# Performance work log

Measured on AMD Instinct MI355X. Metric: run time of the kernel, lower is better.

Reference implementation:

```python
import jax, jax.numpy as jnp
import numpy as np

B, N, K = 32, 1024, 20          # graphs, points per graph, kNN neighbors
EMB = 1024                       # emb_dims
OUT = 7                          # out_channels
WS1, ST1, G1 = 52, 20, 7         # linear1 STFT-KAN: window, stride, gridsize
WS2, ST2, G2 = 197, 7, 6         # linear2 STFT-KAN
NW1 = (128 - WS1) // ST1 + 1     # 4 windows over 128-dim features
NW2 = (2 * EMB - WS2) // ST2 + 1 # 265 windows over 2048-dim features


def _window(kind, M):
    n = jnp.arange(M, dtype=jnp.float32)
    if kind == 'bartlett':
        return 1.0 - jnp.abs(2.0 * n / M - 1.0)        # periodic bartlett (torch default)
    return 0.5 * (1.0 - jnp.cos(2.0 * jnp.pi * n / M)) # periodic hann


def _stft_kan(x, coeffs, bias, gridsize, ws, stride, wtype):
    """x: [B, D]; coeffs: [2, outdim, nw, ws, gridsize]; returns [B, outdim]."""
    D = x.shape[1]
    nw = (D - ws) // stride + 1
    idx = jnp.arange(nw)[:, None] * stride + jnp.arange(ws)[None, :]  # [nw, ws]
    xw = x[:, idx] * _window(wtype, ws)                               # [B, nw, ws]
    kk = jnp.arange(1, gridsize + 1, dtype=x.dtype)
    ang = xw[..., None] * kk                                          # [B, nw, ws, g]
    y = jnp.einsum('bnwg,onwg->bo', jnp.cos(ang), coeffs[0])
    y = y + jnp.einsum('bnwg,onwg->bo', jnp.sin(ang), coeffs[1])
    return y + bias


def setup_inputs() -> dict:
    key = jax.random.key(0)
    ks = jax.random.split(key, 8)
    pos = jax.random.normal(ks[0], (B * N, 3), jnp.float32)
    batch = jnp.repeat(jnp.arange(B, dtype=jnp.int32), N)  # sorted, equal-size graphs
    # EdgeConv MLP([6,64,128]): Linear+BN+ReLU, then plain Linear
    W1 = jax.random.normal(ks[1], (6, 64), jnp.float32) * 0.3
    b1 = jnp.zeros((64,), jnp.float32)
    gamma1 = jnp.ones((64,), jnp.float32)
    beta1 = jnp.zeros((64,), jnp.float32)
    W2 = jax.random.normal(ks[2], (64, 128), jnp.float32) * 0.1
    b2 = jnp.zeros((128,), jnp.float32)
    # STFT-KAN 1 (smooth init: coeffs damped by k^2)
    k1 = np.arange(1, G1 + 1, dtype=np.float32)
    c1 = jax.random.normal(ks[3], (2, EMB, NW1, WS1, G1), jnp.float32) / (np.sqrt(NW1 * WS1) * (k1 ** 2))
    bi1 = jnp.zeros((EMB,), jnp.float32)
    # STFT-KAN 2 (non-smooth init)
    c2 = jax.random.normal(ks[4], (2, OUT, NW2, WS2, G2), jnp.float32) / (np.sqrt(NW2 * WS2) * np.sqrt(G2))
    bi2 = jnp.zeros((OUT,), jnp.float32)
    return {"pos": pos, "batch": batch, "W1": W1, "b1": b1, "gamma1": gamma1,
            "beta1": beta1, "W2": W2, "b2": b2, "c1": c1, "bi1": bi1, "c2": c2, "bi2": bi2}


def reference(pos, batch, W1, b1, gamma1, beta1, W2, b2, c1, bi1, c2, bi2):
    p = pos.reshape(B, N, 3)
    # dynamic kNN graph per batch element (exclude self)
    sq = jnp.sum(p * p, axis=-1)                                    # [B, N]
    d2 = sq[:, :, None] + sq[:, None, :] - 2.0 * jnp.einsum('bnd,bmd->bnm', p, p)
    d2 = d2 + jnp.eye(N, dtype=p.dtype) * 1e10
    _, idx = jax.lax.top_k(-d2, K)                                  # [B, N, K]
    pj = jax.vmap(lambda pts, ids: pts[ids])(p, idx)                # [B, N, K, 3]
    pi = jnp.broadcast_to(p[:, :, None, :], (B, N, K, 3))
    e = jnp.concatenate([pi, pj - pi], axis=-1)                     # [B, N, K, 6]
    # edge MLP: Linear -> BN -> ReLU -> Linear
    h = e @ W1 + b1
    mu = h.mean((0, 1, 2))
    var = h.var((0, 1, 2))
    h = gamma1 * (h - mu) * jax.lax.rsqrt(var + 1e-5) + beta1
    h = jax.nn.relu(h)
    h = h @ W2 + b2                                                 # [B, N, K, 128]
    x1 = h.max(axis=2).reshape(B * N, 128)                          # max aggregation over neighbors
    x = _stft_kan(x1, c1, bi1, G1, WS1, ST1, 'bartlett')            # [B*N, EMB]
    xg = x.reshape(B, N, EMB)
    xcat = jnp.concatenate([xg.max(axis=1), xg.mean(axis=1)], axis=-1)  # global max/mean pool
    return _stft_kan(xcat, c2, bi2, G2, WS2, ST2, 'hann')           # [B, OUT]
```

## Files before the change

kernel.cpp:

```cpp
#include <hip/hip_runtime.h>
#include <cstdint>

typedef _Float16 half8 __attribute__((ext_vector_type(8)));
typedef __fp16 fp16x2 __attribute__((ext_vector_type(2)));
typedef float f32x2 __attribute__((ext_vector_type(2)));
typedef float f32x4 __attribute__((ext_vector_type(4)));

__device__ __forceinline__ void gload16(const void* g, void* l) {
  __builtin_amdgcn_global_load_lds(
      (const __attribute__((address_space(1))) void*)g,
      (__attribute__((address_space(3))) void*)l, 16, 0, 0);
}

__global__ __launch_bounds__(256) void knn_kernel(const float* __restrict__ pos,
                                                  int* __restrict__ nbr) {
  __shared__ float px[1024], py[1024], pz[1024], sq[1024];
  int tid = threadIdx.x;
  int b = blockIdx.x >> 8;
  const float* pg = pos + (size_t)b * 3072;
  for (int m = 0; m < 4; ++m) {
    int j = m * 256 + tid;
    float x = pg[3 * j], y = pg[3 * j + 1], z = pg[3 * j + 2];
    px[j] = x; py[j] = y; pz[j] = z; sq[j] = x * x + y * y + z * z;
  }
  __syncthreads();
  int wave = tid >> 6, lane = tid & 63;
  int n = (blockIdx.x & 255) * 4 + wave;
  float xi = px[n], yi = py[n], zi = pz[n], si = sq[n];
  float d[16];
#pragma unroll
  for (int i = 0; i < 16; ++i) {
    int j = i * 64 + lane;
    float dd = si + sq[j] - 2.0f * (xi * px[j] + yi * py[j] + zi * pz[j]);
    d[i] = (j == n) ? 1e30f : dd;
  }
  int outbase = (b * 1024 + n) * 20;
  for (int kk = 0; kk < 20; ++kk) {
    float lmin = d[0]; int lpos = 0;
#pragma unroll
    for (int i = 1; i < 16; ++i)
      if (d[i] < lmin) { lmin = d[i]; lpos = i; }
    float bv = lmin; int bi = lpos * 64 + lane;
#pragma unroll
    for (int off = 1; off < 64; off <<= 1) {
      float ov = __shfl_xor(bv, off);
      int   oi = __shfl_xor(bi, off);
      if (ov < bv || (ov == bv && oi < bi)) { bv = ov; bi = oi; }
    }
    if (lane == 0) nbr[outbase + kk] = b * 1024 + bi;
    if ((bi & 63) == lane) {
      int rp = bi >> 6;
#pragma unroll
      for (int i = 0; i < 16; ++i)
        if (i == rp) d[i] = 1e30f;
    }
  }
}

__global__ __launch_bounds__(256) void edge_stats_kernel(
    const float* __restrict__ pos, const int* __restrict__ nbr,
    const float* __restrict__ W1, const float* __restrict__ b1v,
    float* __restrict__ psum, float* __restrict__ psq) {
  __shared__ float els[256][6];
  __shared__ float w1s[384];
  __shared__ float b1s[64];
  __shared__ float red[8][64];
  int tid = threadIdx.x, bid = blockIdx.x;
  for (int f = tid; f < 384; f += 256) w1s[f] = W1[f];
  if (tid < 64) b1s[tid] = b1v[tid];
  int c = tid & 63, grp = tid >> 6;
  float s = 0.f, s2 = 0.f;
  for (int ch = 0; ch < 5; ++ch) {
    int E = bid * 1280 + ch * 256 + tid;
    int p = E / 20;
    int j = nbr[E];
    float pix = pos[3 * p], piy = pos[3 * p + 1], piz = pos[3 * p + 2];
    float e3 = pos[3 * j] - pix, e4 = pos[3 * j + 1] - piy, e5 = pos[3 * j + 2] - piz;
    __syncthreads();
    els[tid][0] = pix; els[tid][1] = piy; els[tid][2] = piz;
    els[tid][3] = e3;  els[tid][4] = e4;  els[tid][5] = e5;
    __syncthreads();
    for (int m = 0; m < 64; ++m) {
      int e = grp * 64 + m;
      float h = b1s[c];
#pragma unroll
      for (int d = 0; d < 6; ++d) h += els[e][d] * w1s[d * 64 + c];
      s += h; s2 += h * h;
    }
  }
  red[grp][c] = s;
  __syncthreads();
  red[4 + grp][c] = s2;
  __syncthreads();
  if (tid < 64) {
    float S = red[0][tid] + red[1][tid] + red[2][tid] + red[3][tid];
    float Q = red[4][tid] + red[5][tid] + red[6][tid] + red[7][tid];
    psum[bid * 64 + tid] = S;
    psq[bid * 64 + tid] = Q;
  }
}

__global__ void bn_finalize_kernel(const float* __restrict__ psum, const float* __restrict__ psq,
                                   const float* __restrict__ gamma, const float* __restrict__ beta,
                                   float* __restrict__ bns, float* __restrict__ bnh) {
  int c = threadIdx.x;
  float s = 0.f, q = 0.f;
  for (int b = 0; b < 512; ++b) { s += psum[b * 64 + c]; q += psq[b * 64 + c]; }
  const float inv = 1.0f / 655360.0f;
  float mu = s * inv;
  float var = q * inv - mu * mu;
  float sc = gamma[c] * rsqrtf(var + 1e-5f);
  bns[c] = sc;
  bnh[c] = beta[c] - mu * sc;
}

__global__ __launch_bounds__(256) void edge_mlp_kernel(
    const float* __restrict__ pos, const int* __restrict__ nbr,
    const float* __restrict__ W1, const float* __restrict__ b1v,
    const float* __restrict__ bns, const float* __restrict__ bnh,
    const float* __restrict__ W2, const float* __restrict__ b2v,
    float* __restrict__ x1) {
  __shared__ __align__(16) char elds[53248];
  _Float16* Ah = (_Float16*)(elds);
  _Float16* Al = (_Float16*)(elds + 10240);
  _Float16* Bh = (_Float16*)(elds + 20480);
  _Float16* Bl = (_Float16*)(elds + 36864);
  float* outb = (float*)elds;
  __shared__ float w1s[384];
  __shared__ float b1s[64], scs[64], shs[64];
  int tid = threadIdx.x, bid = blockIdx.x;
  for (int f = tid; f < 384; f += 256) w1s[f] = W1[f];
  if (tid < 64) { b1s[tid] = b1v[tid]; scs[tid] = bns[tid]; shs[tid] = bnh[tid]; }
#pragma unroll
  for (int i = 0; i < 32; ++i) {
    int flat = tid + 256 * i;
    int dd = flat >> 7, c = flat & 127;
    float v = W2[flat];
    _Float16 hi = (_Float16)v;
    _Float16 lo = (_Float16)(v - (float)hi);
    int byte = c * 128 + ((((dd >> 3) ^ (c & 7))) << 4) + (dd & 7) * 2;
    *(_Float16*)((char*)Bh + byte) = hi;
    *(_Float16*)((char*)Bl + byte) = lo;
  }
  __syncthreads();
#pragma unroll
  for (int m = 0; m < 20; ++m) {
    int flat = tid + 256 * m;
    int row = flat >> 6;
    int d = flat & 63;
    int j = nbr[bid * 80 + row];
    int P = bid * 4 + (row / 20);
    float pix = pos[3 * P], piy = pos[3 * P + 1], piz = pos[3 * P + 2];
    float e3 = pos[3 * j] - pix, e4 = pos[3 * j + 1] - piy, e5 = pos[3 * j + 2] - piz;
    float h = b1s[d];
    h += pix * w1s[d] + piy * w1s[64 + d] + piz * w1s[128 + d]
       + e3 * w1s[192 + d] + e4 * w1s[256 + d] + e5 * w1s[320 + d];
    h = scs[d] * h + shs[d];
    h = fmaxf(h, 0.f);
    _Float16 hi = (_Float16)h;
    _Float16 lo = (_Float16)(h - (float)hi);
    int byte = row * 128 + ((((d >> 3) ^ (row & 7))) << 4) + (d & 7) * 2;
    *(_Float16*)((char*)Ah + byte) = hi;
    *(_Float16*)((char*)Al + byte) = lo;
  }
  __syncthreads();
  int wave = tid >> 6, lane = tid & 63;
  int l15 = lane & 15, l4 = lane >> 4;
  f32x4 acc[5][2] = {};
#pragma unroll
  for (int ks = 0; ks < 2; ++ks) {
    int slotk = ks * 4 + l4;
    half8 bfh[2], bfl[2];
#pragma unroll
    for (int ci = 0; ci < 2; ++ci) {
      int col = (wave * 2 + ci) * 16 + l15;
      int byte = col * 128 + ((slotk ^ (col & 7)) << 4);
      bfh[ci] = *(const half8*)((char*)Bh + byte);
      bfl[ci] = *(const half8*)((char*)Bl + byte);
    }
#pragma unroll
    for (int rt = 0; rt < 5; ++rt) {
      int row = rt * 16 + l15;
      int byte = row * 128 + ((slotk ^ (row & 7)) << 4);
      half8 ah = *(const half8*)((char*)Ah + byte);
      half8 al = *(const half8*)((char*)Al + byte);
#pragma unroll
      for (int ci = 0; ci < 2; ++ci) {
        acc[rt][ci] = __builtin_amdgcn_mfma_f32_16x16x32_f16(ah, bfh[ci], acc[rt][ci], 0, 0, 0);
        acc[rt][ci] = __builtin_amdgcn_mfma_f32_16x16x32_f16(ah, bfl[ci], acc[rt][ci], 0, 0, 0);
        acc[rt][ci] = __builtin_amdgcn_mfma_f32_16x16x32_f16(al, bfh[ci], acc[rt][ci], 0, 0, 0);
      }
    }
  }
  __syncthreads();
#pragma unroll
  for (int rt = 0; rt < 5; ++rt)
#pragma unroll
    for (int ci = 0; ci < 2; ++ci) {
      int col = (wave * 2 + ci) * 16 + l15;
#pragma unroll
      for (int q = 0; q < 4; ++q) {
        int row = rt * 16 + l4 * 4 + q;
        outb[row * 129 + col] = acc[rt][ci][q];
      }
    }
  __syncthreads();
#pragma unroll
  for (int r = 0; r < 2; ++r) {
    int it = tid + 256 * r;
    int p = it >> 7, c = it & 127;
    float mx = -1e30f;
#pragma unroll
    for (int e = 0; e < 20; ++e) mx = fmaxf(mx, outb[(p * 20 + e) * 129 + c]);
    x1[((size_t)bid * 4 + p) * 128 + c] = mx + b2v[c];
  }
}

__global__ void c1_to_f16_kernel(const float* __restrict__ c1, _Float16* __restrict__ Cf) {
  int L = blockIdx.x * 256 + threadIdx.x;
  if (L >= 1024 * 3328) return;
  int o = L / 3328, rem = L % 3328;
  int t = rem >> 6, idx = rem & 63;
  int s = idx >> 3, e = idx & 7;
  int half = s >> 2, n = s & 3;
  float v = 0.0f;
  if (!(half == 1 && e >= 6)) {
    int phase = e & 1;
    int g0 = half * 4 + (e >> 1);
    v = c1[((((size_t)phase * 1024 + o) * 4 + n) * 52 + t) * 7 + g0];
  }
  Cf[L] = (_Float16)v;
}

__global__ __launch_bounds__(512, 4) void kan1_gemm_kernel(
    const float* __restrict__ x1, const _Float16* __restrict__ Cf,
    float* __restrict__ pmax, float* __restrict__ psump) {
  __shared__ __align__(16) _Float16 Bsm[2][128 * 64];
  int tid = threadIdx.x;
  int bm = blockIdx.x, bn = blockIdx.y;
  int m0 = bm << 8, n0 = bn << 7;
  int wave = tid >> 6, lane = tid & 63;
  int wr = wave >> 1, wc = wave & 1;
  int l15 = lane & 15, l4 = lane >> 4;

  auto stageB = [&](int t, int nb) {
    int j0 = t << 6;
#pragma unroll
    for (int i = 0; i < 2; ++i) {
      int idx = i * 512 + tid;
      int col = idx >> 3, slot = idx & 7;
      int sslot = slot ^ (col & 7);
      gload16(Cf + (size_t)(n0 + col) * 3328 + j0 + sslot * 8,
              (char*)Bsm[nb] + idx * 16);
    }
  };

  const float* xbase = x1 + (size_t)(m0 + wr * 64 + l15) * 128 + l4 * 20;
  float xr[4];
#pragma unroll
  for (int mi = 0; mi < 4; ++mi) xr[mi] = xbase[mi * 2048];
  stageB(0, 0);
  f32x4 acc[4][4] = {};
  __syncthreads();

  for (int t = 0; t < 52; ++t) {
    int cur = t & 1, nxt = cur ^ 1;
    if (t < 51) stageB(t + 1, nxt);
    float bart = 1.0f - fabsf((float)(2 * t) * (1.0f / 52.0f) - 1.0f);
    half8 a0[4], a1[4];
#pragma unroll
    for (int mi = 0; mi < 4; ++mi) {
      float th = xr[mi] * bart;
      float sn, cs;
      __sincosf(th, &sn, &cs);
      float c2s = cs + cs;
      f32x2 c2v = {c2s, c2s};
      f32x2 p1 = {cs, sn};
      f32x2 p2 = c2v * p1 - (f32x2){1.0f, 0.0f};
      f32x2 p3 = c2v * p2 - p1;
      f32x2 p4 = c2v * p3 - p2;
      f32x2 p5 = c2v * p4 - p3;
      f32x2 p6 = c2v * p5 - p4;
      f32x2 p7 = c2v * p6 - p5;
      union { half8 v; fp16x2 q[4]; } u0, u1;
      u0.q[0] = __builtin_amdgcn_cvt_pkrtz(p1.x, p1.y);
      u0.q[1] = __builtin_amdgcn_cvt_pkrtz(p2.x, p2.y);
      u0.q[2] = __builtin_amdgcn_cvt_pkrtz(p3.x, p3.y);
      u0.q[3] = __builtin_amdgcn_cvt_pkrtz(p4.x, p4.y);
      u1.q[0] = __builtin_amdgcn_cvt_pkrtz(p5.x, p5.y);
      u1.q[1] = __builtin_amdgcn_cvt_pkrtz(p6.x, p6.y);
      u1.q[2] = __builtin_amdgcn_cvt_pkrtz(p7.x, p7.y);
      u1.q[3] = (fp16x2){(__fp16)0.0f, (__fp16)0.0f};
      a0[mi] = u0.v;
      a1[mi] = u1.v;
    }
    if (t < 51) {
#pragma unroll
      for (int mi = 0; mi < 4; ++mi) xr[mi] = xbase[mi * 2048 + t + 1];
    }
    {
      half8 bf[4];
#pragma unroll
      for (int ni = 0; ni < 4; ++ni) {
        int col = wc * 64 + ni * 16 + l15;
        bf[ni] = *(const half8*)((char*)Bsm[cur] + col * 128 + ((l4 ^ (col & 7)) << 4));
      }
#pragma unroll
      for (int mi = 0; mi < 4; ++mi)
#pragma unroll
        for (int ni = 0; ni < 4; ++ni)
          acc[mi][ni] = __builtin_amdgcn_mfma_f32_16x16x32_f16(a0[mi], bf[ni], acc[mi][ni], 0, 0, 0);
    }
    {
      half8 bf[4];
#pragma unroll
      for (int ni = 0; ni < 4; ++ni) {
        int col = wc * 64 + ni * 16 + l15;
        bf[ni] = *(const half8*)((char*)Bsm[cur] + col * 128 + (((4 + l4) ^ (col & 7)) << 4));
      }
#pragma unroll
      for (int mi = 0; mi < 4; ++mi)
#pragma unroll
        for (int ni = 0; ni < 4; ++ni)
          acc[mi][ni] = __builtin_amdgcn_mfma_f32_16x16x32_f16(a1[mi], bf[ni], acc[mi][ni], 0, 0, 0);
    }
    __syncthreads();
  }

  float* pooled = (float*)Bsm;
#pragma unroll
  for (int ni = 0; ni < 4; ++ni) {
    float mx = -1e30f, sm = 0.f;
#pragma unroll
    for (int mi = 0; mi < 4; ++mi)
#pragma unroll
      for (int q = 0; q < 4; ++q) {
        float v = acc[mi][ni][q];
        mx = fmaxf(mx, v); sm += v;
      }
    mx = fmaxf(mx, __shfl_xor(mx, 16)); sm += __shfl_xor(sm, 16);
    mx = fmaxf(mx, __shfl_xor(mx, 32)); sm += __shfl_xor(sm, 32);
    if (l4 == 0) {
      int col = wc * 64 + ni * 16 + l15;
      pooled[(wr * 2 + 0) * 128 + col] = mx;
      pooled[(wr * 2 + 1) * 128 + col] = sm;
    }
  }
  __syncthreads();
  if (tid < 128) {
    float mx = pooled[tid], sm = pooled[128 + tid];
#pragma unroll
    for (int w = 1; w < 4; ++w) {
      mx = fmaxf(mx, pooled[(w * 2 + 0) * 128 + tid]);
      sm += pooled[(w * 2 + 1) * 128 + tid];
    }
    pmax[(size_t)bm * 1024 + n0 + tid] = mx;
    psump[(size_t)bm * 1024 + n0 + tid] = sm;
  }
}

__global__ void pool_reduce_kernel(const float* __restrict__ pmax, const float* __restrict__ psump,
                                   const float* __restrict__ bi1,
                                   float* __restrict__ gmax, float* __restrict__ gmean) {
  int gid = blockIdx.x * 256 + threadIdx.x;
  int b = gid >> 10, col = gid & 1023;
  float mx = -1e30f, sm = 0.f;
  for (int t = 0; t < 4; ++t) {
    mx = fmaxf(mx, pmax[(size_t)(b * 4 + t) * 1024 + col]);
    sm += psump[(size_t)(b * 4 + t) * 1024 + col];
  }
  float bias = bi1[col];
  gmax[gid] = mx + bias;
  gmean[gid] = sm * (1.0f / 1024.0f) + bias;
}

__global__ __launch_bounds__(256) void kan2_kernel(
    const float* __restrict__ gmax, const float* __restrict__ gmean,
    const float* __restrict__ c2, float* __restrict__ part) {
  __shared__ float xc[2048];
  __shared__ float hw[197];
  __shared__ float racc[7][256];
  int b = blockIdx.x, s = blockIdx.y, tid = threadIdx.x;
  for (int f = tid; f < 1024; f += 256) {
    xc[f] = gmax[b * 1024 + f];
    xc[1024 + f] = gmean[b * 1024 + f];
  }
  for (int f = tid; f < 197; f += 256)
    hw[f] = 0.5f * (1.0f - cosf(6.283185307179586f * (float)f / 197.0f));
  float acc[7] = {};
  __syncthreads();
  int qlo = (52205 * s) / 16, qhi = (52205 * (s + 1)) / 16;
  for (int q = qlo + tid; q < qhi; q += 256) {
    int n = q / 197;
    int w = q - n * 197;
    float xw = xc[n * 7 + w] * hw[w];
    float s1, c1v;
    __sincosf(xw, &s1, &c1v);
    float ckv[6], skv[6];
    {
      float ck = c1v, sk = s1;
#pragma unroll
      for (int g = 0; g < 6; ++g) {
        ckv[g] = ck; skv[g] = sk;
        float cn = ck * c1v - sk * s1;
        sk = sk * c1v + ck * s1;
        ck = cn;
      }
    }
    int base = q * 6;
#pragma unroll
    for (int o = 0; o < 7; ++o) {
      const float* pc = c2 + (size_t)o * 313230 + base;
      const float* ps = c2 + (size_t)(o + 7) * 313230 + base;
      float sc = 0.f, ss = 0.f;
#pragma unroll
      for (int g = 0; g < 6; ++g) { sc += ckv[g] * pc[g]; ss += skv[g] * ps[g]; }
      acc[o] += sc + ss;
    }
  }
#pragma unroll
  for (int o = 0; o < 7; ++o) racc[o][tid] = acc[o];
  __syncthreads();
  for (int st = 128; st >= 1; st >>= 1) {
    if (tid < st)
#pragma unroll
      for (int o = 0; o < 7; ++o) racc[o][tid] += racc[o][tid + st];
    __syncthreads();
  }
  if (tid < 7) part[(b * 16 + s) * 7 + tid] = racc[tid][0];
}

__global__ void kan2_reduce_kernel(const float* __restrict__ part, const float* __restrict__ bi2,
                                   float* __restrict__ out) {
  int i = threadIdx.x;
  if (i >= 224) return;
  int b = i / 7, o = i % 7;
  float s = 0.f;
  for (int t = 0; t < 16; ++t) s += part[(b * 16 + t) * 7 + o];
  out[b * 7 + o] = s + bi2[o];
}

extern "C" void kernel_launch(void* const* d_in, const int* in_sizes, int n_in,
                              void* d_out, int out_size, void* d_ws, size_t ws_size,
                              hipStream_t stream) {
  const float* pos    = (const float*)d_in[0];
  const float* W1     = (const float*)d_in[2];
  const float* b1     = (const float*)d_in[3];
  const float* gamma1 = (const float*)d_in[4];
  const float* beta1  = (const float*)d_in[5];
  const float* W2     = (const float*)d_in[6];
  const float* b2     = (const float*)d_in[7];
  const float* c1     = (const float*)d_in[8];
  const float* bi1    = (const float*)d_in[9];
  const float* c2     = (const float*)d_in[10];
  const float* bi2    = (const float*)d_in[11];
  float* out = (float*)d_out;
  char* ws = (char*)d_ws;

  int*      nbr   = (int*)     (ws + 0);
  float*    x1    = (float*)   (ws + 2621440);
  _Float16* Cf    = (_Float16*)(ws + 19398656);
  float*    psum  = (float*)   (ws + 26214400);
  float*    psq   = (float*)   (ws + 26345472);
  float*    bns   = (float*)   (ws + 26476544);
  float*    bnh   = (float*)   (ws + 26476800);
  float*    pmax  = (float*)   (ws + 26477056);
  float*    psump = (float*)   (ws + 27001344);
  float*    gmax  = (float*)   (ws + 27525632);
  float*    gmean = (float*)   (ws + 27656704);
  float*    part  = (float*)   (ws + 27787776);
  if (ws_size < 27802112) return;

  knn_kernel<<<8192, 256, 0, stream>>>(pos, nbr);
  c1_to_f16_kernel<<<13312, 256, 0, stream>>>(c1, Cf);
  edge_stats_kernel<<<512, 256, 0, stream>>>(pos, nbr, W1, b1, psum, psq);
  bn_finalize_kernel<<<1, 64, 0, stream>>>(psum, psq, gamma1, beta1, bns, bnh);
  edge_mlp_kernel<<<8192, 256, 0, stream>>>(pos, nbr, W1, b1, bns, bnh, W2, b2, x1);
  kan1_gemm_kernel<<<dim3(128, 8), 512, 0, stream>>>(x1, Cf, pmax, psump);
  pool_reduce_kernel<<<128, 256, 0, stream>>>(pmax, psump, bi1, gmax, gmean);
  kan2_kernel<<<dim3(32, 16), 256, 0, stream>>>(gmax, gmean, c2, part);
  kan2_reduce_kernel<<<1, 256, 0, stream>>>(part, bi2, out);
}
```

Before: 593.1 us.

## Use DPP reductions in kNN argmin and stage two taps per KAN1 GEMM iteration

```diff
diff --git a/kernel.cpp b/kernel.cpp
--- a/kernel.cpp
+++ b/kernel.cpp
@@ -10,6 +10,16 @@
   __builtin_amdgcn_global_load_lds(
       (const __attribute__((address_space(1))) void*)g,
       (__attribute__((address_space(3))) void*)l, 16, 0, 0);
+}
+
+template <int CTRL, int RM>
+__device__ __forceinline__ void dppmin(float& d, int& j) {
+  int di = __builtin_amdgcn_update_dpp(__float_as_int(d), __float_as_int(d), CTRL, RM, 0xf, false);
+  int ji = __builtin_amdgcn_update_dpp(j, j, CTRL, RM, 0xf, false);
+  float df = __int_as_float(di);
+  bool c = (df < d) || (df == d && ji < j);
+  d = c ? df : d;
+  j = c ? ji : j;
 }
 
 __global__ __launch_bounds__(256) void knn_kernel(const float* __restrict__ pos,
@@ -41,15 +51,16 @@
     for (int i = 1; i < 16; ++i)
       if (d[i] < lmin) { lmin = d[i]; lpos = i; }
     float bv = lmin; int bi = lpos * 64 + lane;
-#pragma unroll
-    for (int off = 1; off < 64; off <<= 1) {
-      float ov = __shfl_xor(bv, off);
-      int   oi = __shfl_xor(bi, off);
-      if (ov < bv || (ov == bv && oi < bi)) { bv = ov; bi = oi; }
-    }
-    if (lane == 0) nbr[outbase + kk] = b * 1024 + bi;
-    if ((bi & 63) == lane) {
-      int rp = bi >> 6;
+    dppmin<0xB1, 0xf>(bv, bi);
+    dppmin<0x4E, 0xf>(bv, bi);
+    dppmin<0x141, 0xf>(bv, bi);
+    dppmin<0x140, 0xf>(bv, bi);
+    dppmin<0x142, 0xa>(bv, bi);
+    dppmin<0x143, 0xc>(bv, bi);
+    int widx = __builtin_amdgcn_readlane(bi, 63);
+    if (lane == 0) nbr[outbase + kk] = b * 1024 + widx;
+    if ((widx & 63) == lane) {
+      int rp = widx >> 6;
 #pragma unroll
       for (int i = 0; i < 16; ++i)
         if (i == rp) d[i] = 1e30f;
@@ -84,7 +95,7 @@
       int e = grp * 64 + m;
       float h = b1s[c];
 #pragma unroll
-      for (int d = 0; d < 6; ++d) h += els[e][d] * w1s[d * 64 + c];
+      for (int dd = 0; dd < 6; ++dd) h += els[e][dd] * w1s[dd * 64 + c];
       s += h; s2 += h * h;
     }
   }
@@ -235,7 +246,7 @@
 __global__ __launch_bounds__(512, 4) void kan1_gemm_kernel(
     const float* __restrict__ x1, const _Float16* __restrict__ Cf,
     float* __restrict__ pmax, float* __restrict__ psump) {
-  __shared__ __align__(16) _Float16 Bsm[2][128 * 64];
+  __shared__ __align__(16) _Float16 Bsm[2][128 * 128];
   int tid = threadIdx.x;
   int bm = blockIdx.x, bn = blockIdx.y;
   int m0 = bm << 8, n0 = bn << 7;
@@ -243,86 +254,100 @@
   int wr = wave >> 1, wc = wave & 1;
   int l15 = lane & 15, l4 = lane >> 4;
 
-  auto stageB = [&](int t, int nb) {
-    int j0 = t << 6;
-#pragma unroll
-    for (int i = 0; i < 2; ++i) {
-      int idx = i * 512 + tid;
-      int col = idx >> 3, slot = idx & 7;
-      int sslot = slot ^ (col & 7);
-      gload16(Cf + (size_t)(n0 + col) * 3328 + j0 + sslot * 8,
-              (char*)Bsm[nb] + idx * 16);
-    }
+  auto stageB = [&](int i, int nb) {
+    int j0 = i << 7;
+#pragma unroll
+    for (int tt = 0; tt < 2; ++tt)
+#pragma unroll
+      for (int ii = 0; ii < 2; ++ii) {
+        int idx = ii * 512 + tid;
+        int col = idx >> 3, slot = idx & 7;
+        int sslot = slot ^ (col & 7);
+        gload16(Cf + (size_t)(n0 + col) * 3328 + j0 + tt * 64 + sslot * 8,
+                (char*)Bsm[nb] + tt * 16384 + idx * 16);
+      }
   };
+  auto agen = [&](float xv, float bart, half8& o0, half8& o1) {
+    float th = xv * bart;
+    float sn, cs;
+    __sincosf(th, &sn, &cs);
+    float c2s = cs + cs;
+    f32x2 c2v = {c2s, c2s};
+    f32x2 p1 = {cs, sn};
+    f32x2 p2 = c2v * p1 - (f32x2){1.0f, 0.0f};
+    f32x2 p3 = c2v * p2 - p1;
+    f32x2 p4 = c2v * p3 - p2;
+    f32x2 p5 = c2v * p4 - p3;
+    f32x2 p6 = c2v * p5 - p4;
+    f32x2 p7 = c2v * p6 - p5;
+    union { half8 v; fp16x2 q[4]; } u0, u1;
+    u0.q[0] = __builtin_amdgcn_cvt_pkrtz(p1.x, p1.y);
+    u0.q[1] = __builtin_amdgcn_cvt_pkrtz(p2.x, p2.y);
+    u0.q[2] = __builtin_amdgcn_cvt_pkrtz(p3.x, p3.y);
+    u0.q[3] = __builtin_amdgcn_cvt_pkrtz(p4.x, p4.y);
+    u1.q[0] = __builtin_amdgcn_cvt_pkrtz(p5.x, p5.y);
+    u1.q[1] = __builtin_amdgcn_cvt_pkrtz(p6.x, p6.y);
+    u1.q[2] = __builtin_amdgcn_cvt_pkrtz(p7.x, p7.y);
+    u1.q[3] = (fp16x2){(__fp16)0.0f, (__fp16)0.0f};
+    o0 = u0.v;
+    o1 = u1.v;
+  };
+  auto mfma_tap = [&](int nb, int tt, half8* a0, half8* a1, f32x4 (*acc)[4]) {
+    half8 bf[4];
+#pragma unroll
+    for (int ni = 0; ni < 4; ++ni) {
+      int col = wc * 64 + ni * 16 + l15;
+      bf[ni] = *(const half8*)((char*)Bsm[nb] + tt * 16384 + col * 128 + ((l4 ^ (col & 7)) << 4));
+    }
+#pragma unroll
+    for (int mi = 0; mi < 4; ++mi)
+#pragma unroll
+      for (int ni = 0; ni < 4; ++ni)
+        acc[mi][ni] = __builtin_amdgcn_mfma_f32_16x16x32_f16(a0[mi], bf[ni], acc[mi][ni], 0, 0, 0);
+#pragma unroll
+    for (int ni = 0; ni < 4; ++ni) {
+      int col = wc * 64 + ni * 16 + l15;
+      bf[ni] = *(const half8*)((char*)Bsm[nb] + tt * 16384 + col * 128 + (((4 + l4) ^ (col & 7)) << 4));
+    }
+#pragma unroll
+    for (int mi = 0; mi < 4; ++mi)
+#pragma unroll
+      for (int ni = 0; ni < 4; ++ni)
+        acc[mi][ni] = __builtin_amdgcn_mfma_f32_16x16x32_f16(a1[mi], bf[ni], acc[mi][ni], 0, 0, 0);
+  };
 
   const float* xbase = x1 + (size_t)(m0 + wr * 64 + l15) * 128 + l4 * 20;
-  float xr[4];
-#pragma unroll
-  for (int mi = 0; mi < 4; ++mi) xr[mi] = xbase[mi * 2048];
+  float xa[4], xb[4];
+#pragma unroll
+  for (int mi = 0; mi < 4; ++mi) { xa[mi] = xbase[mi * 2048]; xb[mi] = xbase[mi * 2048 + 1]; }
   stageB(0, 0);
   f32x4 acc[4][4] = {};
   __syncthreads();
 
-  for (int t = 0; t < 52; ++t) {
-    int cur = t & 1, nxt = cur ^ 1;
-    if (t < 51) stageB(t + 1, nxt);
-    float bart = 1.0f - fabsf((float)(2 * t) * (1.0f / 52.0f) - 1.0f);
-    half8 a0[4], a1[4];
-#pragma unroll
-    for (int mi = 0; mi < 4; ++mi) {
-      float th = xr[mi] * bart;
-      float sn, cs;
-      __sincosf(th, &sn, &cs);
-      float c2s = cs + cs;
-      f32x2 c2v = {c2s, c2s};
-      f32x2 p1 = {cs, sn};
-      f32x2 p2 = c2v * p1 - (f32x2){1.0f, 0.0f};
-      f32x2 p3 = c2v * p2 - p1;
-      f32x2 p4 = c2v * p3 - p2;
-      f32x2 p5 = c2v * p4 - p3;
-      f32x2 p6 = c2v * p5 - p4;
-      f32x2 p7 = c2v * p6 - p5;
-      union { half8 v; fp16x2 q[4]; } u0, u1;
-      u0.q[0] = __builtin_amdgcn_cvt_pkrtz(p1.x, p1.y);
-      u0.q[1] = __builtin_amdgcn_cvt_pkrtz(p2.x, p2.y);
-      u0.q[2] = __builtin_amdgcn_cvt_pkrtz(p3.x, p3.y);
-      u0.q[3] = __builtin_amdgcn_cvt_pkrtz(p4.x, p4.y);
-      u1.q[0] = __builtin_amdgcn_cvt_pkrtz(p5.x, p5.y);
-      u1.q[1] = __builtin_amdgcn_cvt_pkrtz(p6.x, p6.y);
-      u1.q[2] = __builtin_amdgcn_cvt_pkrtz(p7.x, p7.y);
-      u1.q[3] = (fp16x2){(__fp16)0.0f, (__fp16)0.0f};
-      a0[mi] = u0.v;
-      a1[mi] = u1.v;
-    }
-    if (t < 51) {
-#pragma unroll
-      for (int mi = 0; mi < 4; ++mi) xr[mi] = xbase[mi * 2048 + t + 1];
-    }
+  for (int i = 0; i < 26; ++i) {
+    int cur = i & 1, nxt = cur ^ 1;
+    if (i < 25) stageB(i + 1, nxt);
     {
-      half8 bf[4];
-#pragma unroll
-      for (int ni = 0; ni < 4; ++ni) {
-        int col = wc * 64 + ni * 16 + l15;
-        bf[ni] = *(const half8*)((char*)Bsm[cur] + col * 128 + ((l4 ^ (col & 7)) << 4));
-      }
-#pragma unroll
-      for (int mi = 0; mi < 4; ++mi)
-#pragma unroll
-        for (int ni = 0; ni < 4; ++ni)
-          acc[mi][ni] = __builtin_amdgcn_mfma_f32_16x16x32_f16(a0[mi], bf[ni], acc[mi][ni], 0, 0, 0);
+      float bart = 1.0f - fabsf((float)(4 * i) * (1.0f / 52.0f) - 1.0f);
+      half8 a0[4], a1[4];
+#pragma unroll
+      for (int mi = 0; mi < 4; ++mi) agen(xa[mi], bart, a0[mi], a1[mi]);
+      if (i < 25) {
+#pragma unroll
+        for (int mi = 0; mi < 4; ++mi) xa[mi] = xbase[mi * 2048 + 2 * i + 2];
+      }
+      mfma_tap(cur, 0, a0, a1, acc);
     }
     {
-      half8 bf[4];
-#pragma unroll
-      for (int ni = 0; ni < 4; ++ni) {
-        int col = wc * 64 + ni * 16 + l15;
-        bf[ni] = *(const half8*)((char*)Bsm[cur] + col * 128 + (((4 + l4) ^ (col & 7)) << 4));
-      }
-#pragma unroll
-      for (int mi = 0; mi < 4; ++mi)
-#pragma unroll
-        for (int ni = 0; ni < 4; ++ni)
-          acc[mi][ni] = __builtin_amdgcn_mfma_f32_16x16x32_f16(a1[mi], bf[ni], acc[mi][ni], 0, 0, 0);
+      float bart = 1.0f - fabsf((float)(4 * i + 2) * (1.0f / 52.0f) - 1.0f);
+      half8 a0[4], a1[4];
+#pragma unroll
+      for (int mi = 0; mi < 4; ++mi) agen(xb[mi], bart, a0[mi], a1[mi]);
+      if (i < 25) {
+#pragma unroll
+        for (int mi = 0; mi < 4; ++mi) xb[mi] = xbase[mi * 2048 + 2 * i + 3];
+      }
+      mfma_tap(cur, 1, a0, a1, acc);
     }
     __syncthreads();
   }
```

After: 771.7 us. +30.1%, slower.
